# Kernel optimization log

Measured on AMD Instinct MI355X. Metric: run time of the kernel, lower is better.

The kernel has to match this reference:

```python
import jax, jax.numpy as jnp
import numpy as np

DIM = 256
P = 0.1            # trainable-drop-rate
TEMP = 0.2         # trainable-temp
K = round(DIM * P) # number of peeling iterations (26)


def setup_inputs() -> dict:
    key = jax.random.key(0)
    k1, k2, k3 = jax.random.split(key, 3)
    N = 300000
    feature = jax.random.normal(k1, (N, DIM), dtype=jnp.float32)
    # Linear(dim, dim) params; scaled like torch default init (~1/sqrt(dim))
    W = jax.random.normal(k2, (DIM, DIM), dtype=jnp.float32) / jnp.sqrt(DIM)
    b = jax.random.normal(k3, (DIM,), dtype=jnp.float32) / jnp.sqrt(DIM)
    return {"feature": feature, "W": W, "b": b}


def reference(feature, W, b):
    # mask = Linear(feature)
    mask = feature @ W.T + b  # [N, dim]

    def step(y, _):
        w = 1.0 - y                              # remaining (un-dropped) weight
        logits = (mask + jnp.log(w + 1e-12)) / TEMP
        y1 = jax.nn.softmax(logits, axis=1)      # stable: subtracts row max
        return y + y1 * w, None

    y, _ = jax.lax.scan(step, jnp.zeros_like(mask), None, length=K)
    soft_mask = (1.0 - y) / (1.0 - P)
    return feature * soft_mask
```

## Files before the change

### kernel.cpp

```cpp
#include <hip/hip_runtime.h>
#include <hip/hip_bf16.h>
#include <math.h>

typedef _Float16 f16x8 __attribute__((ext_vector_type(8)));
typedef _Float16 f16x4 __attribute__((ext_vector_type(4)));
typedef float    f32x4 __attribute__((ext_vector_type(4)));
typedef float    f32x2 __attribute__((ext_vector_type(2)));

#define DIMD    256
#define MT      64
#define BT      256
#define KSTEPS  26
#define EXP_C   7.2134752044448170f
#define LOG2E   1.4426950408889634f
#define INV_1MP 1.1111111111111112f

static __device__ __forceinline__ f32x2 pk_fma(f32x2 a, f32x2 b, f32x2 c) {
    f32x2 d;
    asm("v_pk_fma_f32 %0, %1, %2, %3" : "=v"(d) : "v"(a), "v"(b), "v"(c));
    return d;
}
static __device__ __forceinline__ f32x2 pk_mul(f32x2 a, f32x2 b) {
    f32x2 d;
    asm("v_pk_mul_f32 %0, %1, %2" : "=v"(d) : "v"(a), "v"(b));
    return d;
}
static __device__ __forceinline__ f32x2 pk_add(f32x2 a, f32x2 b) {
    f32x2 d;
    asm("v_pk_add_f32 %0, %1, %2" : "=v"(d) : "v"(a), "v"(b));
    return d;
}

template<int CTRL>
static __device__ __forceinline__ float dpp_ror(float s) {
    return __builtin_bit_cast(float, __builtin_amdgcn_update_dpp(
        0, __builtin_bit_cast(int, s), CTRL, 0xf, 0xf, false));
}
static __device__ __forceinline__ float row16_sum(float s) {
    s += dpp_ror<0x128>(s);
    s += dpp_ror<0x124>(s);
    s += dpp_ror<0x122>(s);
    s += dpp_ror<0x121>(s);
    return s;
}
static __device__ __forceinline__ float row16_max(float m) {
    m = fmaxf(m, dpp_ror<0x128>(m));
    m = fmaxf(m, dpp_ror<0x124>(m));
    m = fmaxf(m, dpp_ror<0x122>(m));
    m = fmaxf(m, dpp_ror<0x121>(m));
    return m;
}

__global__ __launch_bounds__(256)
void w_conv_kernel(const float* __restrict__ W, f16x8* __restrict__ ws) {
    int gid  = blockIdx.x * 256 + threadIdx.x;
    int tile = gid >> 6;
    int lane = gid & 63;
    int kt = tile >> 4, ct = tile & 15;
    int col = ct * 16 + (lane & 15);
    int k0  = kt * 32 + (lane >> 4) * 8;
    const float* wr = W + col * 256 + k0;
    float4 f01 = *(const float4*)wr;
    float4 f23 = *(const float4*)(wr + 4);
    float wv[8] = {f01.x, f01.y, f01.z, f01.w, f23.x, f23.y, f23.z, f23.w};
    f16x8 hi;
    #pragma unroll
    for (int j = 0; j < 8; ++j) hi[j] = (_Float16)wv[j];
    ws[tile * 64 + lane] = hi;
}

__global__ __launch_bounds__(BT, 4)
void sad_mfma_kernel(const float* __restrict__ feat,
                     const float* __restrict__ bias,
                     const f16x8* __restrict__ ws,
                     float* __restrict__ out,
                     int N)
{
    __shared__ __align__(16) unsigned char smem[MT * 512];

    const int tid  = threadIdx.x;
    const int lane = tid & 63;
    const int wv   = tid >> 6;
    const long long n0 = (long long)blockIdx.x * MT;

    const float4* fvec = (const float4*)feat;
    #pragma unroll
    for (int i = 0; i < 16; ++i) {
        int flat4 = i * BT + tid;
        int row = flat4 >> 6;
        int c4  = flat4 & 63;
        long long grow = n0 + row;
        if (grow >= N) grow = N - 1;
        float4 f = fvec[grow * 64 + c4];
        f16x4 h4;
        h4[0] = (_Float16)f.x; h4[1] = (_Float16)f.y;
        h4[2] = (_Float16)f.z; h4[3] = (_Float16)f.w;
        int off = row * 512 + ((c4 * 8) ^ ((row & 7) << 4));
        *(f16x4*)(smem + off) = h4;
    }
    __syncthreads();

    f32x4 acc[16];
    #pragma unroll
    for (int ct = 0; ct < 16; ++ct) {
        float b = bias[ct * 16 + (lane & 15)];
        acc[ct] = f32x4{b, b, b, b};
    }

    const int arow  = wv * 16 + (lane & 15);
    const int swzA  = (arow & 7) << 4;
    const int abase = arow * 512;
    const int kgrp  = (lane >> 4) * 16;

    #pragma unroll
    for (int kt = 0; kt < 8; ++kt) {
        int kbyte = kt * 64 + kgrp;
        f16x8 a8 = *(const f16x8*)(smem + abase + (kbyte ^ swzA));
        #pragma unroll
        for (int ct = 0; ct < 16; ++ct) {
            f16x8 bh = ws[(kt * 16 + ct) * 64 + lane];
            acc[ct] = __builtin_amdgcn_mfma_f32_16x16x32_f16(a8, bh, acc[ct], 0, 0, 0);
        }
    }

    float M[4];
    #pragma unroll
    for (int p = 0; p < 4; ++p) {
        float m = acc[0][p];
        #pragma unroll
        for (int ct = 1; ct < 16; ++ct) m = fmaxf(m, acc[ct][p]);
        M[p] = row16_max(m);
    }

    const f32x2 one2 = f32x2{1.0f, 1.0f};

    #pragma unroll 1
    for (int p = 0; p < 4; ++p) {
        f32x2 q[8];
        #pragma unroll
        for (int cc = 0; cc < 8; ++cc) {
            q[cc] = f32x2{
                __builtin_amdgcn_exp2f((acc[2 * cc][p]     - M[p]) * EXP_C),
                __builtin_amdgcn_exp2f((acc[2 * cc + 1][p] - M[p]) * EXP_C)};
        }

        #pragma unroll 1
        for (int it = 0; it < KSTEPS; ++it) {
            f32x2 s2 = pk_add(pk_add(pk_add(q[0], q[1]), pk_add(q[2], q[3])),
                              pk_add(pk_add(q[4], q[5]), pk_add(q[6], q[7])));
            float s = row16_sum(s2.x + s2.y);
            s = fmaxf(s, 1e-30f);
            float nr = -__builtin_amdgcn_rcpf(s);
            f32x2 nrv = f32x2{nr, nr};
            #pragma unroll
            for (int cc = 0; cc < 8; ++cc) {
                f32x2 r  = pk_fma(q[cc], nrv, one2);
                f32x2 r2 = pk_mul(r, r);
                f32x2 r4 = pk_mul(r2, r2);
                f32x2 r5 = pk_mul(r4, r);
                q[cc] = pk_mul(q[cc], r5);
            }
        }

        int row = wv * 16 + (lane >> 4) * 4 + p;
        long long grow = n0 + row;
        if (grow < N) {
            int swz = (row & 7) << 4;
            float* orow = out + grow * 256;
            #pragma unroll
            for (int cc = 0; cc < 8; ++cc) {
                #pragma unroll
                for (int h = 0; h < 2; ++h) {
                    int col = (2 * cc + h) * 16 + (lane & 15);
                    float le5 = (acc[2 * cc + h][p] - M[p]) * LOG2E;
                    float qv  = fmaxf(h ? q[cc].y : q[cc].x, 1e-38f);
                    float zz  = __builtin_amdgcn_exp2f(
                        fmaf(__builtin_amdgcn_logf(qv), 0.2f, -le5));
                    int off = row * 512 + ((col * 2) ^ swz);
                    float fval = (float)(*(const _Float16*)(smem + off));
                    orow[col] = fval * (zz * INV_1MP);
                }
            }
        }
    }
}

extern "C" void kernel_launch(void* const* d_in, const int* in_sizes, int n_in,
                              void* d_out, int out_size, void* d_ws, size_t ws_size,
                              hipStream_t stream) {
    const float* feat = (const float*)d_in[0];
    const float* W    = (const float*)d_in[1];
    const float* bias = (const float*)d_in[2];
    float* out = (float*)d_out;
    int N = in_sizes[0] / DIMD;

    w_conv_kernel<<<32, 256, 0, stream>>>(W, (f16x8*)d_ws);

    int grid = (int)((N + MT - 1) / MT);
    sad_mfma_kernel<<<grid, BT, 0, stream>>>(feat, bias, (const f16x8*)d_ws, out, N);
}
```

Measured before the change: 327.9 us.

## Split GEMM and peeling into separate kernels via fp16 logit workspace

```diff
diff --git a/kernel.cpp b/kernel.cpp
--- a/kernel.cpp
+++ b/kernel.cpp
@@ -4,6 +4,7 @@
 
 typedef _Float16 f16x8 __attribute__((ext_vector_type(8)));
 typedef _Float16 f16x4 __attribute__((ext_vector_type(4)));
+typedef _Float16 f16x2 __attribute__((ext_vector_type(2)));
 typedef float    f32x4 __attribute__((ext_vector_type(4)));
 typedef float    f32x2 __attribute__((ext_vector_type(2)));
 
@@ -14,6 +15,10 @@
 #define EXP_C   7.2134752044448170f
 #define LOG2E   1.4426950408889634f
 #define INV_1MP 1.1111111111111112f
+
+static __device__ __forceinline__ f16x2 cvt_pk(float a, float b) {
+    return __builtin_bit_cast(f16x2, __builtin_amdgcn_cvt_pkrtz(a, b));
+}
 
 static __device__ __forceinline__ f32x2 pk_fma(f32x2 a, f32x2 b, f32x2 c) {
     f32x2 d;
@@ -70,17 +75,16 @@
 }
 
 __global__ __launch_bounds__(BT, 4)
-void sad_mfma_kernel(const float* __restrict__ feat,
+void sad_gemm_kernel(const float* __restrict__ feat,
                      const float* __restrict__ bias,
                      const f16x8* __restrict__ ws,
-                     float* __restrict__ out,
-                     int N)
+                     unsigned int* __restrict__ lew,
+                     int N, int totThreads)
 {
     __shared__ __align__(16) unsigned char smem[MT * 512];
 
     const int tid  = threadIdx.x;
     const int lane = tid & 63;
-    const int wv   = tid >> 6;
     const long long n0 = (long long)blockIdx.x * MT;
 
     const float4* fvec = (const float4*)feat;
@@ -107,6 +111,7 @@
         acc[ct] = f32x4{b, b, b, b};
     }
 
+    const int wv    = tid >> 6;
     const int arow  = wv * 16 + (lane & 15);
     const int swzA  = (arow & 7) << 4;
     const int abase = arow * 512;
@@ -123,26 +128,49 @@
         }
     }
 
-    float M[4];
+    long long gtid = (long long)blockIdx.x * BT + tid;
     #pragma unroll
     for (int p = 0; p < 4; ++p) {
         float m = acc[0][p];
         #pragma unroll
         for (int ct = 1; ct < 16; ++ct) m = fmaxf(m, acc[ct][p]);
-        M[p] = row16_max(m);
-    }
-
+        float M = row16_max(m);
+        #pragma unroll
+        for (int cc = 0; cc < 8; ++cc) {
+            f16x2 le = cvt_pk((acc[2 * cc][p]     - M) * LOG2E,
+                              (acc[2 * cc + 1][p] - M) * LOG2E);
+            lew[(long long)(p * 8 + cc) * totThreads + gtid] =
+                __builtin_bit_cast(unsigned int, le);
+        }
+    }
+}
+
+__global__ __launch_bounds__(BT, 8)
+void sad_peel_kernel(const float* __restrict__ feat,
+                     const unsigned int* __restrict__ lew,
+                     float* __restrict__ out,
+                     int N, int totThreads)
+{
+    const int tid  = threadIdx.x;
+    const int lane = tid & 63;
+    const int wv   = tid >> 6;
+    const long long n0 = (long long)blockIdx.x * MT;
+    const long long gtid = (long long)blockIdx.x * BT + tid;
     const f32x2 one2 = f32x2{1.0f, 1.0f};
 
     #pragma unroll 1
     for (int p = 0; p < 4; ++p) {
+        f16x2 lp[8];
+        #pragma unroll
+        for (int cc = 0; cc < 8; ++cc)
+            lp[cc] = __builtin_bit_cast(f16x2,
+                lew[(long long)(p * 8 + cc) * totThreads + gtid]);
+
         f32x2 q[8];
         #pragma unroll
-        for (int cc = 0; cc < 8; ++cc) {
-            q[cc] = f32x2{
-                __builtin_amdgcn_exp2f((acc[2 * cc][p]     - M[p]) * EXP_C),
-                __builtin_amdgcn_exp2f((acc[2 * cc + 1][p] - M[p]) * EXP_C)};
-        }
+        for (int cc = 0; cc < 8; ++cc)
+            q[cc] = f32x2{__builtin_amdgcn_exp2f(5.0f * (float)lp[cc][0]),
+                          __builtin_amdgcn_exp2f(5.0f * (float)lp[cc][1])};
 
         #pragma unroll 1
         for (int it = 0; it < KSTEPS; ++it) {
@@ -162,6 +190,112 @@
             }
         }
 
+        int row = wv * 16 + (lane >> 4) * 4 + p;
+        long long grow = n0 + row;
+        if (grow < N) {
+            const float* frow = feat + grow * 256;
+            float* orow = out + grow * 256;
+            #pragma unroll
+            for (int cc = 0; cc < 8; ++cc) {
+                #pragma unroll
+                for (int h = 0; h < 2; ++h) {
+                    int col = (2 * cc + h) * 16 + (lane & 15);
+                    float le5 = (float)lp[cc][h];
+                    float qv  = fmaxf(h ? q[cc].y : q[cc].x, 1e-38f);
+                    float zz  = __builtin_amdgcn_exp2f(
+                        fmaf(__builtin_amdgcn_logf(qv), 0.2f, -le5));
+                    orow[col] = frow[col] * (zz * INV_1MP);
+                }
+            }
+        }
+    }
+}
+
+__global__ __launch_bounds__(BT, 4)
+void sad_fused_kernel(const float* __restrict__ feat,
+                      const float* __restrict__ bias,
+                      const f16x8* __restrict__ ws,
+                      float* __restrict__ out,
+                      int N)
+{
+    __shared__ __align__(16) unsigned char smem[MT * 512];
+    const int tid  = threadIdx.x;
+    const int lane = tid & 63;
+    const int wv   = tid >> 6;
+    const long long n0 = (long long)blockIdx.x * MT;
+
+    const float4* fvec = (const float4*)feat;
+    #pragma unroll
+    for (int i = 0; i < 16; ++i) {
+        int flat4 = i * BT + tid;
+        int row = flat4 >> 6;
+        int c4  = flat4 & 63;
+        long long grow = n0 + row;
+        if (grow >= N) grow = N - 1;
+        float4 f = fvec[grow * 64 + c4];
+        f16x4 h4;
+        h4[0] = (_Float16)f.x; h4[1] = (_Float16)f.y;
+        h4[2] = (_Float16)f.z; h4[3] = (_Float16)f.w;
+        int off = row * 512 + ((c4 * 8) ^ ((row & 7) << 4));
+        *(f16x4*)(smem + off) = h4;
+    }
+    __syncthreads();
+
+    f32x4 acc[16];
+    #pragma unroll
+    for (int ct = 0; ct < 16; ++ct) {
+        float b = bias[ct * 16 + (lane & 15)];
+        acc[ct] = f32x4{b, b, b, b};
+    }
+    const int arow  = wv * 16 + (lane & 15);
+    const int swzA  = (arow & 7) << 4;
+    const int abase = arow * 512;
+    const int kgrp  = (lane >> 4) * 16;
+    #pragma unroll
+    for (int kt = 0; kt < 8; ++kt) {
+        int kbyte = kt * 64 + kgrp;
+        f16x8 a8 = *(const f16x8*)(smem + abase + (kbyte ^ swzA));
+        #pragma unroll
+        for (int ct = 0; ct < 16; ++ct) {
+            f16x8 bh = ws[(kt * 16 + ct) * 64 + lane];
+            acc[ct] = __builtin_amdgcn_mfma_f32_16x16x32_f16(a8, bh, acc[ct], 0, 0, 0);
+        }
+    }
+    float M[4];
+    #pragma unroll
+    for (int p = 0; p < 4; ++p) {
+        float m = acc[0][p];
+        #pragma unroll
+        for (int ct = 1; ct < 16; ++ct) m = fmaxf(m, acc[ct][p]);
+        M[p] = row16_max(m);
+    }
+    const f32x2 one2 = f32x2{1.0f, 1.0f};
+    #pragma unroll 1
+    for (int p = 0; p < 4; ++p) {
+        f32x2 q[8];
+        #pragma unroll
+        for (int cc = 0; cc < 8; ++cc) {
+            q[cc] = f32x2{
+                __builtin_amdgcn_exp2f((acc[2 * cc][p]     - M[p]) * EXP_C),
+                __builtin_amdgcn_exp2f((acc[2 * cc + 1][p] - M[p]) * EXP_C)};
+        }
+        #pragma unroll 1
+        for (int it = 0; it < KSTEPS; ++it) {
+            f32x2 s2 = pk_add(pk_add(pk_add(q[0], q[1]), pk_add(q[2], q[3])),
+                              pk_add(pk_add(q[4], q[5]), pk_add(q[6], q[7])));
+            float s = row16_sum(s2.x + s2.y);
+            s = fmaxf(s, 1e-30f);
+            float nr = -__builtin_amdgcn_rcpf(s);
+            f32x2 nrv = f32x2{nr, nr};
+            #pragma unroll
+            for (int cc = 0; cc < 8; ++cc) {
+                f32x2 r  = pk_fma(q[cc], nrv, one2);
+                f32x2 r2 = pk_mul(r, r);
+                f32x2 r4 = pk_mul(r2, r2);
+                f32x2 r5 = pk_mul(r4, r);
+                q[cc] = pk_mul(q[cc], r5);
+            }
+        }
         int row = wv * 16 + (lane >> 4) * 4 + p;
         long long grow = n0 + row;
         if (grow < N) {
@@ -193,9 +327,19 @@
     const float* bias = (const float*)d_in[2];
     float* out = (float*)d_out;
     int N = in_sizes[0] / DIMD;
+    int grid = (N + MT - 1) / MT;
+    long long totThreads = (long long)grid * BT;
 
     w_conv_kernel<<<32, 256, 0, stream>>>(W, (f16x8*)d_ws);
 
-    int grid = (int)((N + MT - 1) / MT);
-    sad_mfma_kernel<<<grid, BT, 0, stream>>>(feat, bias, (const f16x8*)d_ws, out, N);
-}
+    size_t need = (size_t)131072 + (size_t)totThreads * 32u * 4u;
+    if (ws_size >= need) {
+        unsigned int* lew = (unsigned int*)((unsigned char*)d_ws + 131072);
+        sad_gemm_kernel<<<grid, BT, 0, stream>>>(feat, bias, (const f16x8*)d_ws,
+                                                 lew, N, (int)totThreads);
+        sad_peel_kernel<<<grid, BT, 0, stream>>>(feat, lew, out, N, (int)totThreads);
+    } else {
+        sad_fused_kernel<<<grid, BT, 0, stream>>>(feat, bias, (const f16x8*)d_ws,
+                                                  out, N);
+    }
+}
```

Measured after the change: 443.5 us. 1.35x slower.

## Chunk GEMM into packed fp16 logits and interleave four rows in peeling loop

Applied to the files above, without the earlier changes.

```diff
diff --git a/kernel.cpp b/kernel.cpp
--- a/kernel.cpp
+++ b/kernel.cpp
@@ -4,6 +4,7 @@
 
 typedef _Float16 f16x8 __attribute__((ext_vector_type(8)));
 typedef _Float16 f16x4 __attribute__((ext_vector_type(4)));
+typedef _Float16 f16x2 __attribute__((ext_vector_type(2)));
 typedef float    f32x4 __attribute__((ext_vector_type(4)));
 typedef float    f32x2 __attribute__((ext_vector_type(2)));
 
@@ -11,9 +12,12 @@
 #define MT      64
 #define BT      256
 #define KSTEPS  26
-#define EXP_C   7.2134752044448170f
 #define LOG2E   1.4426950408889634f
 #define INV_1MP 1.1111111111111112f
+
+static __device__ __forceinline__ f16x2 cvt_pk(float a, float b) {
+    return __builtin_bit_cast(f16x2, __builtin_amdgcn_cvt_pkrtz(a, b));
+}
 
 static __device__ __forceinline__ f32x2 pk_fma(f32x2 a, f32x2 b, f32x2 c) {
     f32x2 d;
@@ -42,13 +46,6 @@
     s += dpp_ror<0x122>(s);
     s += dpp_ror<0x121>(s);
     return s;
-}
-static __device__ __forceinline__ float row16_max(float m) {
-    m = fmaxf(m, dpp_ror<0x128>(m));
-    m = fmaxf(m, dpp_ror<0x124>(m));
-    m = fmaxf(m, dpp_ror<0x122>(m));
-    m = fmaxf(m, dpp_ror<0x121>(m));
-    return m;
 }
 
 __global__ __launch_bounds__(256)
@@ -69,6 +66,33 @@
     ws[tile * 64 + lane] = hi;
 }
 
+#define GEMM_CHUNK(C)                                                         \
+{                                                                             \
+    f32x4 acc[4];                                                             \
+    _Pragma("unroll")                                                         \
+    for (int t = 0; t < 4; ++t) {                                             \
+        float b = bias[(4 * (C) + t) * 16 + (lane & 15)];                     \
+        acc[t] = f32x4{b, b, b, b};                                           \
+    }                                                                         \
+    _Pragma("unroll")                                                         \
+    for (int kt = 0; kt < 8; ++kt) {                                          \
+        int kbyte = kt * 64 + kgrp;                                           \
+        f16x8 a8 = *(const f16x8*)(smem + abase + (kbyte ^ swzA));            \
+        _Pragma("unroll")                                                     \
+        for (int t = 0; t < 4; ++t) {                                         \
+            f16x8 bh = ws[(kt * 16 + 4 * (C) + t) * 64 + lane];               \
+            acc[t] = __builtin_amdgcn_mfma_f32_16x16x32_f16(a8, bh,           \
+                                                            acc[t], 0, 0, 0); \
+        }                                                                     \
+    }                                                                         \
+    _Pragma("unroll")                                                         \
+    for (int p = 0; p < 4; ++p) {                                             \
+        le[C][p][0] = cvt_pk(acc[0][p] * LOG2E, acc[1][p] * LOG2E);           \
+        le[C][p][1] = cvt_pk(acc[2][p] * LOG2E, acc[3][p] * LOG2E);           \
+        asm volatile("" : "+v"(le[C][p][0]), "+v"(le[C][p][1]));              \
+    }                                                                         \
+}
+
 __global__ __launch_bounds__(BT, 4)
 void sad_mfma_kernel(const float* __restrict__ feat,
                      const float* __restrict__ bias,
@@ -100,68 +124,62 @@
     }
     __syncthreads();
 
-    f32x4 acc[16];
-    #pragma unroll
-    for (int ct = 0; ct < 16; ++ct) {
-        float b = bias[ct * 16 + (lane & 15)];
-        acc[ct] = f32x4{b, b, b, b};
-    }
-
     const int arow  = wv * 16 + (lane & 15);
     const int swzA  = (arow & 7) << 4;
     const int abase = arow * 512;
     const int kgrp  = (lane >> 4) * 16;
 
-    #pragma unroll
-    for (int kt = 0; kt < 8; ++kt) {
-        int kbyte = kt * 64 + kgrp;
-        f16x8 a8 = *(const f16x8*)(smem + abase + (kbyte ^ swzA));
-        #pragma unroll
-        for (int ct = 0; ct < 16; ++ct) {
-            f16x8 bh = ws[(kt * 16 + ct) * 64 + lane];
-            acc[ct] = __builtin_amdgcn_mfma_f32_16x16x32_f16(a8, bh, acc[ct], 0, 0, 0);
-        }
-    }
-
-    float M[4];
+    f16x2 le[4][4][2];
+    GEMM_CHUNK(0)
+    asm volatile("" ::: "memory");
+    GEMM_CHUNK(1)
+    asm volatile("" ::: "memory");
+    GEMM_CHUNK(2)
+    asm volatile("" ::: "memory");
+    GEMM_CHUNK(3)
+    asm volatile("" ::: "memory");
+
+    const f32x2 one2 = f32x2{1.0f, 1.0f};
+
+    f32x2 q[4][8];
     #pragma unroll
     for (int p = 0; p < 4; ++p) {
-        float m = acc[0][p];
-        #pragma unroll
-        for (int ct = 1; ct < 16; ++ct) m = fmaxf(m, acc[ct][p]);
-        M[p] = row16_max(m);
-    }
-
-    const f32x2 one2 = f32x2{1.0f, 1.0f};
-
-    #pragma unroll 1
-    for (int p = 0; p < 4; ++p) {
-        f32x2 q[8];
         #pragma unroll
         for (int cc = 0; cc < 8; ++cc) {
-            q[cc] = f32x2{
-                __builtin_amdgcn_exp2f((acc[2 * cc][p]     - M[p]) * EXP_C),
-                __builtin_amdgcn_exp2f((acc[2 * cc + 1][p] - M[p]) * EXP_C)};
-        }
-
-        #pragma unroll 1
-        for (int it = 0; it < KSTEPS; ++it) {
-            f32x2 s2 = pk_add(pk_add(pk_add(q[0], q[1]), pk_add(q[2], q[3])),
-                              pk_add(pk_add(q[4], q[5]), pk_add(q[6], q[7])));
+            q[p][cc] = f32x2{
+                __builtin_amdgcn_exp2f(5.0f * (float)le[cc >> 1][p][cc & 1][0]),
+                __builtin_amdgcn_exp2f(5.0f * (float)le[cc >> 1][p][cc & 1][1])};
+        }
+    }
+
+    #pragma unroll 1
+    for (int it = 0; it < KSTEPS; ++it) {
+        f32x2 nrv[4];
+        #pragma unroll
+        for (int p = 0; p < 4; ++p) {
+            f32x2 s2 = pk_add(
+                pk_add(pk_add(q[p][0], q[p][1]), pk_add(q[p][2], q[p][3])),
+                pk_add(pk_add(q[p][4], q[p][5]), pk_add(q[p][6], q[p][7])));
             float s = row16_sum(s2.x + s2.y);
             s = fmaxf(s, 1e-30f);
             float nr = -__builtin_amdgcn_rcpf(s);
-            f32x2 nrv = f32x2{nr, nr};
+            nrv[p] = f32x2{nr, nr};
+        }
+        #pragma unroll
+        for (int cc = 0; cc < 8; ++cc) {
             #pragma unroll
-            for (int cc = 0; cc < 8; ++cc) {
-                f32x2 r  = pk_fma(q[cc], nrv, one2);
+            for (int p = 0; p < 4; ++p) {
+                f32x2 r  = pk_fma(q[p][cc], nrv[p], one2);
                 f32x2 r2 = pk_mul(r, r);
                 f32x2 r4 = pk_mul(r2, r2);
                 f32x2 r5 = pk_mul(r4, r);
-                q[cc] = pk_mul(q[cc], r5);
+                q[p][cc] = pk_mul(q[p][cc], r5);
             }
         }
-
+    }
+
+    #pragma unroll
+    for (int p = 0; p < 4; ++p) {
         int row = wv * 16 + (lane >> 4) * 4 + p;
         long long grow = n0 + row;
         if (grow < N) {
@@ -172,8 +190,8 @@
                 #pragma unroll
                 for (int h = 0; h < 2; ++h) {
                     int col = (2 * cc + h) * 16 + (lane & 15);
-                    float le5 = (acc[2 * cc + h][p] - M[p]) * LOG2E;
-                    float qv  = fmaxf(h ? q[cc].y : q[cc].x, 1e-38f);
+                    float le5 = (float)le[cc >> 1][p][cc & 1][h];
+                    float qv  = fmaxf(h ? q[p][cc].y : q[p][cc].x, 1e-38f);
                     float zz  = __builtin_amdgcn_exp2f(
                         fmaf(__builtin_amdgcn_logf(qv), 0.2f, -le5));
                     int off = row * 512 + ((col * 2) ^ swz);
@@ -196,6 +214,6 @@
 
     w_conv_kernel<<<32, 256, 0, stream>>>(W, (f16x8*)d_ws);
 
-    int grid = (int)((N + MT - 1) / MT);
+    int grid = (N + MT - 1) / MT;
     sad_mfma_kernel<<<grid, BT, 0, stream>>>(feat, bias, (const f16x8*)d_ws, out, N);
 }
```

Result: slower. 438.1 us (+33.6%).
